# Kernel tuning notes

Measured on AMD Instinct MI355X. Metric: run time of the kernel, lower is better.

## Reference

```python
import jax, jax.numpy as jnp
import numpy as np

# Module constants (from init_kwargs)
P = 10000          # query points
G = 6400           # gaussians
C = 18             # semantic classes
H, W, D = 200, 200, 16
GRID = 0.5
SCALE_MULT = 3.0
PC_MIN = jnp.array([-50.0, -50.0, -5.0], dtype=jnp.float32)
COV_IDX = np.array([0, 4, 8, 1, 5, 2])  # xx, yy, zz, xy, yz, xz of flattened 3x3


def setup_inputs() -> dict:
    key = jax.random.key(0)
    k1, k2, k3, k4, k5, k6 = jax.random.split(key, 6)
    extent = jnp.array([H, W, D], jnp.float32) * GRID  # [100, 100, 8] meters
    eps = 1e-3  # keep strictly inside grid so int voxel coords are in-range
    pts = PC_MIN + jax.random.uniform(k1, (1, P, 3), jnp.float32) * (extent - eps)
    means3D = PC_MIN + jax.random.uniform(k2, (1, G, 3), jnp.float32) * (extent - eps)
    opacities = jax.random.uniform(k3, (1, G), jnp.float32)
    semantics = jax.random.normal(k4, (1, G, C), jnp.float32)
    # scales in [0.2, 1.0] m -> radii = ceil(max_scale*3/0.5) >= 2 (assert radii >= 1)
    scales = 0.2 + 0.8 * jax.random.uniform(k5, (1, G, 3), jnp.float32)
    # cov3D is the (symmetric PD) precision matrix: R diag(1/s^2) R^T
    A = jax.random.normal(k6, (1, G, 3, 3), jnp.float32)
    Q, _ = jnp.linalg.qr(A)
    inv_var = 1.0 / (scales ** 2)
    cov3D = jnp.einsum('bgij,bgj,bgkj->bgik', Q, inv_var, Q)
    return dict(pts=pts, means3D=means3D, opacities=opacities,
                semantics=semantics, scales=scales, cov3D=cov3D)


def reference(pts, means3D, opacities, semantics, scales, cov3D):
    # squeeze batch dim (module asserts batch == 1)
    p = pts[0]                     # [P,3]
    mu = means3D[0]                # [G,3]
    op = opacities[0]              # [G]
    sem = semantics[0]             # [G,C]
    sc = scales[0]                 # [G,3]
    cov = cov3D[0].reshape(G, 9)[:, COV_IDX]  # [G,6]: xx,yy,zz,xy,yz,xz

    # integer voxel coords (cast truncates; coords are non-negative in-range)
    p_int = ((p - PC_MIN) / GRID).astype(jnp.int32)                              # [P,3]
    m_int = ((jax.lax.stop_gradient(mu) - PC_MIN) / GRID).astype(jnp.int32)      # [G,3]
    radii = jnp.ceil(sc.max(-1) * SCALE_MULT / GRID).astype(jnp.int32)           # [G]

    # voxel-box test: point voxel within per-axis radius of gaussian voxel
    mask = (jnp.abs(p_int[:, None, :] - m_int[None, :, :]) <= radii[None, :, None]).all(-1)  # [P,G]

    # Mahalanobis power with precision matrix entries
    d = p[:, None, :] - mu[None, :, :]           # [P,G,3]
    dx, dy, dz = d[..., 0], d[..., 1], d[..., 2]
    power = (-0.5 * (cov[None, :, 0] * dx * dx
                     + cov[None, :, 1] * dy * dy
                     + cov[None, :, 2] * dz * dz)
             - cov[None, :, 3] * dx * dy
             - cov[None, :, 4] * dy * dz
             - cov[None, :, 5] * dx * dz)        # [P,G]

    w = jnp.where(mask, jnp.exp(power) * op[None, :], 0.0)  # [P,G]
    logits = w @ sem                                         # [P,C]
    return logits
```

## Files before the change

kernel.cpp:

```cpp
#include <hip/hip_runtime.h>
#include <math.h>

#define P_TOTAL 10000
#define G_TOTAL 6400
#define C_CLS   18
#define CS_SH   3
#define NCX     25
#define NCELL   (NCX * NCX)
#define BCAP    256
#define PCAP    96
#define NTHR    512

__global__ void __launch_bounds__(NTHR)
la_cell2(const float* __restrict__ pts,
         const float* __restrict__ means3D,
         const float* __restrict__ opacities,
         const float* __restrict__ semantics,
         const float* __restrict__ scales,
         const float* __restrict__ cov3D,
         float* __restrict__ out) {
    __shared__ int4 sbox[BCAP];
    __shared__ int  splist[PCAP];
    __shared__ int  snb, snp;

    const int t = threadIdx.x;
    const int cell = blockIdx.x;
    const int ccx = cell % NCX;
    const int ccy = cell / NCX;

    if (t == 0) { snb = 0; snp = 0; }
    __syncthreads();

    const float4* p4 = (const float4*)pts;
    for (int j = t; j < P_TOTAL / 4; j += NTHR) {
        float4 a = p4[j * 3 + 0];
        float4 b = p4[j * 3 + 1];
        float4 c = p4[j * 3 + 2];
        float pxs[4] = {a.x, a.w, b.z, c.y};
        float pys[4] = {a.y, b.x, b.w, c.z};
#pragma unroll
        for (int q = 0; q < 4; ++q) {
            int cx = ((int)((pxs[q] + 50.0f) * 2.0f)) >> CS_SH;
            int cy = ((int)((pys[q] + 50.0f) * 2.0f)) >> CS_SH;
            if (cx == ccx && cy == ccy) {
                int s = atomicAdd(&snp, 1);
                if (s < PCAP) splist[s] = j * 4 + q;
            }
        }
    }

    const float4* m4 = (const float4*)means3D;
    const float4* s4 = (const float4*)scales;
    for (int j = t; j < G_TOTAL / 4; j += NTHR) {
        float4 ma = m4[j * 3 + 0], mb = m4[j * 3 + 1], mc = m4[j * 3 + 2];
        float4 sa = s4[j * 3 + 0], sb = s4[j * 3 + 1], sc = s4[j * 3 + 2];
        float mxs[4] = {ma.x, ma.w, mb.z, mc.y};
        float mys[4] = {ma.y, mb.x, mb.w, mc.z};
        float mzs[4] = {ma.z, mb.y, mc.x, mc.w};
        float sxs[4] = {sa.x, sa.w, sb.z, sc.y};
        float sys[4] = {sa.y, sb.x, sb.w, sc.z};
        float szs[4] = {sa.z, sb.y, sc.x, sc.w};
#pragma unroll
        for (int q = 0; q < 4; ++q) {
            int mix = (int)((mxs[q] + 50.0f) * 2.0f);
            int miy = (int)((mys[q] + 50.0f) * 2.0f);
            int miz = (int)((mzs[q] + 5.0f) * 2.0f);
            int r = (int)ceilf((fmaxf(fmaxf(sxs[q], sys[q]), szs[q]) * 3.0f) * 2.0f);
            int w = 2 * r;
            int minx = mix - r, miny = miy - r, minz = miz - r;
            int cx0 = max(minx, 0) >> CS_SH;
            int cx1 = min(minx + w, 199) >> CS_SH;
            int cy0 = max(miny, 0) >> CS_SH;
            int cy1 = min(miny + w, 199) >> CS_SH;
            if (ccx >= cx0 && ccx <= cx1 && ccy >= cy0 && ccy <= cy1) {
                int s = atomicAdd(&snb, 1);
                if (s < BCAP)
                    sbox[s] = make_int4(minx, miny, minz, (w << 16) | (j * 4 + q));
            }
        }
    }
    __syncthreads();

    const int np = min(snp, PCAP);
    const int nb = min(snb, BCAP);
    const int wv = t >> 6, lane = t & 63;

    for (int idx = wv; idx < np; idx += NTHR / 64) {
        int pt = splist[idx];
        float px = pts[pt * 3 + 0];
        float py = pts[pt * 3 + 1];
        float pz = pts[pt * 3 + 2];
        int pix = (int)((px + 50.0f) * 2.0f);
        int piy = (int)((py + 50.0f) * 2.0f);
        int piz = (int)((pz + 5.0f) * 2.0f);

        float acc = 0.0f;
        for (int base = 0; base < nb; base += 64) {
            int i = base + lane;
            float wgt = 0.0f;
            int gid = 0;
            if (i < nb) {
                int4 b = sbox[i];
                unsigned w  = ((unsigned)b.w) >> 16;
                unsigned ux = (unsigned)(pix - b.x);
                unsigned uy = (unsigned)(piy - b.y);
                unsigned uz = (unsigned)(piz - b.z);
                if (ux <= w && uy <= w && uz <= w) {
                    gid = b.w & 0xffff;
                    float mx = means3D[gid * 3 + 0];
                    float my = means3D[gid * 3 + 1];
                    float mz = means3D[gid * 3 + 2];
                    const float* cv = cov3D + (size_t)gid * 9;
                    float dx = px - mx, dy = py - my, dz = pz - mz;
                    float pw = -0.5f * (cv[0] * dx * dx + cv[4] * dy * dy + cv[8] * dz * dz)
                               - cv[1] * dx * dy - cv[5] * dy * dz - cv[2] * dx * dz;
                    wgt = __expf(pw) * opacities[gid];
                }
            }
            unsigned long long m = __ballot(wgt != 0.0f);
            while (m) {
                int h = (int)__builtin_ctzll(m);
                m &= m - 1;
                float wh = __shfl(wgt, h, 64);
                int   gh = __shfl(gid, h, 64);
                if (lane < C_CLS)
                    acc = fmaf(wh, semantics[(size_t)gh * C_CLS + lane], acc);
            }
        }

        if (lane < C_CLS)
            out[(size_t)pt * C_CLS + lane] = acc;
    }
}

extern "C" void kernel_launch(void* const* d_in, const int* in_sizes, int n_in,
                              void* d_out, int out_size, void* d_ws, size_t ws_size,
                              hipStream_t stream) {
    const float* pts      = (const float*)d_in[0];
    const float* means3D  = (const float*)d_in[1];
    const float* opac     = (const float*)d_in[2];
    const float* sem      = (const float*)d_in[3];
    const float* scales   = (const float*)d_in[4];
    const float* cov3D    = (const float*)d_in[5];
    float* out = (float*)d_out;

    la_cell2<<<NCELL, NTHR, 0, stream>>>(pts, means3D, opac, sem, scales, cov3D, out);
}
```

Before: 30.02 us.

## Process four spatial cells per block to amortize global point and gaussian scans

Each block now handles four consecutive grid cells instead of one, so the full scan over all points and gaussians used for binning is shared across four cells. This cuts the redundant global reads, which each block previously repeated over the entire input, by a factor of four. Fewer blocks (157 vs 625) are launched, which reduces parallelism across the GPU's compute units, and the per-cell capacities shrink (BCAP 192, PCAP 64), raising the chance of silently dropping points or gaussians in dense cells.

```diff
diff --git a/kernel.cpp b/kernel.cpp
--- a/kernel.cpp
+++ b/kernel.cpp
@@ -7,29 +7,37 @@
 #define CS_SH   3
 #define NCX     25
 #define NCELL   (NCX * NCX)
-#define BCAP    256
-#define PCAP    96
+#define CPB     4
+#define NBLK    ((NCELL + CPB - 1) / CPB)
+#define BCAP    192
+#define PCAP    64
 #define NTHR    512
 
 __global__ void __launch_bounds__(NTHR)
-la_cell2(const float* __restrict__ pts,
+la_cell4(const float* __restrict__ pts,
          const float* __restrict__ means3D,
          const float* __restrict__ opacities,
          const float* __restrict__ semantics,
          const float* __restrict__ scales,
          const float* __restrict__ cov3D,
          float* __restrict__ out) {
-    __shared__ int4 sbox[BCAP];
-    __shared__ int  splist[PCAP];
-    __shared__ int  snb, snp;
+    __shared__ int4 sbox[CPB][BCAP];
+    __shared__ int  splist[CPB][PCAP];
+    __shared__ int  snb[CPB], snp[CPB];
 
     const int t = threadIdx.x;
-    const int cell = blockIdx.x;
-    const int ccx = cell % NCX;
-    const int ccy = cell / NCX;
+    const int base = blockIdx.x * CPB;
 
-    if (t == 0) { snb = 0; snp = 0; }
+    if (t < CPB) { snb[t] = 0; snp[t] = 0; }
     __syncthreads();
+
+    int ccx[CPB], ccy[CPB];
+#pragma unroll
+    for (int c = 0; c < CPB; ++c) {
+        int cell = base + c;
+        ccy[c] = cell / NCX;
+        ccx[c] = cell - ccy[c] * NCX;
+    }
 
     const float4* p4 = (const float4*)pts;
     for (int j = t; j < P_TOTAL / 4; j += NTHR) {
@@ -42,9 +50,10 @@
         for (int q = 0; q < 4; ++q) {
             int cx = ((int)((pxs[q] + 50.0f) * 2.0f)) >> CS_SH;
             int cy = ((int)((pys[q] + 50.0f) * 2.0f)) >> CS_SH;
-            if (cx == ccx && cy == ccy) {
-                int s = atomicAdd(&snp, 1);
-                if (s < PCAP) splist[s] = j * 4 + q;
+            int rel = cy * NCX + cx - base;
+            if ((unsigned)rel < CPB) {
+                int s = atomicAdd(&snp[rel], 1);
+                if (s < PCAP) splist[rel][s] = j * 4 + q;
             }
         }
     }
@@ -72,64 +81,71 @@
             int cx1 = min(minx + w, 199) >> CS_SH;
             int cy0 = max(miny, 0) >> CS_SH;
             int cy1 = min(miny + w, 199) >> CS_SH;
-            if (ccx >= cx0 && ccx <= cx1 && ccy >= cy0 && ccy <= cy1) {
-                int s = atomicAdd(&snb, 1);
-                if (s < BCAP)
-                    sbox[s] = make_int4(minx, miny, minz, (w << 16) | (j * 4 + q));
+            int4 e = make_int4(minx, miny, minz, (w << 16) | (j * 4 + q));
+#pragma unroll
+            for (int c = 0; c < CPB; ++c) {
+                if (base + c < NCELL &&
+                    ccx[c] >= cx0 && ccx[c] <= cx1 &&
+                    ccy[c] >= cy0 && ccy[c] <= cy1) {
+                    int s = atomicAdd(&snb[c], 1);
+                    if (s < BCAP) sbox[c][s] = e;
+                }
             }
         }
     }
     __syncthreads();
 
-    const int np = min(snp, PCAP);
-    const int nb = min(snb, BCAP);
     const int wv = t >> 6, lane = t & 63;
 
-    for (int idx = wv; idx < np; idx += NTHR / 64) {
-        int pt = splist[idx];
-        float px = pts[pt * 3 + 0];
-        float py = pts[pt * 3 + 1];
-        float pz = pts[pt * 3 + 2];
-        int pix = (int)((px + 50.0f) * 2.0f);
-        int piy = (int)((py + 50.0f) * 2.0f);
-        int piz = (int)((pz + 5.0f) * 2.0f);
+    for (int c = 0; c < CPB; ++c) {
+        const int np = min(snp[c], PCAP);
+        const int nb = min(snb[c], BCAP);
+        for (int idx = wv; idx < np; idx += NTHR / 64) {
+            int pt = splist[c][idx];
+            float px = pts[pt * 3 + 0];
+            float py = pts[pt * 3 + 1];
+            float pz = pts[pt * 3 + 2];
+            int pix = (int)((px + 50.0f) * 2.0f);
+            int piy = (int)((py + 50.0f) * 2.0f);
+            int piz = (int)((pz + 5.0f) * 2.0f);
 
-        float acc = 0.0f;
-        for (int base = 0; base < nb; base += 64) {
-            int i = base + lane;
-            float wgt = 0.0f;
-            int gid = 0;
-            if (i < nb) {
-                int4 b = sbox[i];
-                unsigned w  = ((unsigned)b.w) >> 16;
-                unsigned ux = (unsigned)(pix - b.x);
-                unsigned uy = (unsigned)(piy - b.y);
-                unsigned uz = (unsigned)(piz - b.z);
-                if (ux <= w && uy <= w && uz <= w) {
-                    gid = b.w & 0xffff;
-                    float mx = means3D[gid * 3 + 0];
-                    float my = means3D[gid * 3 + 1];
-                    float mz = means3D[gid * 3 + 2];
-                    const float* cv = cov3D + (size_t)gid * 9;
-                    float dx = px - mx, dy = py - my, dz = pz - mz;
-                    float pw = -0.5f * (cv[0] * dx * dx + cv[4] * dy * dy + cv[8] * dz * dz)
-                               - cv[1] * dx * dy - cv[5] * dy * dz - cv[2] * dx * dz;
-                    wgt = __expf(pw) * opacities[gid];
+            float acc = 0.0f;
+            for (int bse = 0; bse < nb; bse += 64) {
+                int i = bse + lane;
+                float wgt = 0.0f;
+                int gid = 0;
+                if (i < nb) {
+                    int4 b = sbox[c][i];
+                    unsigned w  = ((unsigned)b.w) >> 16;
+                    unsigned ux = (unsigned)(pix - b.x);
+                    unsigned uy = (unsigned)(piy - b.y);
+                    unsigned uz = (unsigned)(piz - b.z);
+                    if (ux <= w && uy <= w && uz <= w) {
+                        gid = b.w & 0xffff;
+                        float mx = means3D[gid * 3 + 0];
+                        float my = means3D[gid * 3 + 1];
+                        float mz = means3D[gid * 3 + 2];
+                        const float* cv = cov3D + (size_t)gid * 9;
+                        float dx = px - mx, dy = py - my, dz = pz - mz;
+                        float pw = -0.5f * (cv[0] * dx * dx + cv[4] * dy * dy + cv[8] * dz * dz)
+                                   - cv[1] * dx * dy - cv[5] * dy * dz - cv[2] * dx * dz;
+                        wgt = __expf(pw) * opacities[gid];
+                    }
+                }
+                unsigned long long m = __ballot(wgt != 0.0f);
+                while (m) {
+                    int h = (int)__builtin_ctzll(m);
+                    m &= m - 1;
+                    float wh = __shfl(wgt, h, 64);
+                    int   gh = __shfl(gid, h, 64);
+                    if (lane < C_CLS)
+                        acc = fmaf(wh, semantics[(size_t)gh * C_CLS + lane], acc);
                 }
             }
-            unsigned long long m = __ballot(wgt != 0.0f);
-            while (m) {
-                int h = (int)__builtin_ctzll(m);
-                m &= m - 1;
-                float wh = __shfl(wgt, h, 64);
-                int   gh = __shfl(gid, h, 64);
-                if (lane < C_CLS)
-                    acc = fmaf(wh, semantics[(size_t)gh * C_CLS + lane], acc);
-            }
+
+            if (lane < C_CLS)
+                out[(size_t)pt * C_CLS + lane] = acc;
         }
-
-        if (lane < C_CLS)
-            out[(size_t)pt * C_CLS + lane] = acc;
     }
 }
 
@@ -144,5 +160,5 @@
     const float* cov3D    = (const float*)d_in[5];
     float* out = (float*)d_out;
 
-    la_cell2<<<NCELL, NTHR, 0, stream>>>(pts, means3D, opac, sem, scales, cov3D, out);
+    la_cell4<<<NBLK, NTHR, 0, stream>>>(pts, means3D, opac, sem, scales, cov3D, out);
 }
```

Result: slower. 48.72 us (+62.3%).
